# Performance work log

Measured on AMD Instinct MI355X. Metric: run time of the kernel, lower is better.

The kernel has to match this reference:

```python
import jax, jax.numpy as jnp
import numpy as np

N_DETS = 50000
DEG = 32
N_EDGES = N_DETS * DEG

def _xavier(key, fan_in, fan_out):
    lim = np.sqrt(6.0 / (fan_in + fan_out)).astype(np.float32)
    return jax.random.uniform(key, (fan_in, fan_out), jnp.float32, -lim, lim)

def setup_inputs() -> dict:
    key = jax.random.key(0)
    ks = jax.random.split(key, 10)
    detFeatures = jax.random.normal(ks[0], (N_DETS, 128), jnp.float32)
    # every detection has exactly DEG neighbor pairs -> sorted segment ids, no empty segments
    cIdxs = jnp.repeat(jnp.arange(N_DETS, dtype=jnp.int64), DEG)
    nIdxs = jax.random.randint(ks[1], (N_EDGES,), 0, N_DETS, jnp.int64)
    pairFeatures = jax.random.normal(ks[2], (N_EDGES, 32), jnp.float32)
    return {
        "detFeatures": detFeatures,
        "cIdxs": cIdxs,
        "nIdxs": nIdxs,
        "pairFeatures": pairFeatures,
        "W_fc1": _xavier(ks[3], 128, 32), "b_fc1": jnp.zeros((32,), jnp.float32),
        "W_pw1": _xavier(ks[4], 96, 64), "b_pw1": jnp.zeros((64,), jnp.float32),
        "W_pw2": _xavier(ks[5], 64, 64), "b_pw2": jnp.zeros((64,), jnp.float32),
        "W_pm1": _xavier(ks[6], 64, 64), "b_pm1": jnp.zeros((64,), jnp.float32),
        "W_pm2": _xavier(ks[7], 64, 64), "b_pm2": jnp.zeros((64,), jnp.float32),
        "W_out": _xavier(ks[8], 64, 128), "b_out": jnp.zeros((128,), jnp.float32),
    }

def reference(detFeatures, cIdxs, nIdxs, pairFeatures,
              W_fc1, b_fc1, W_pw1, b_pw1, W_pw2, b_pw2,
              W_pm1, b_pm1, W_pm2, b_pm2, W_out, b_out):
    relu = jax.nn.relu
    # fc1: [N,128] -> [N,32]
    h = relu(detFeatures @ W_fc1 + b_fc1)
    # gather center / neighbor feats per pair; zero neighbor feats on identity rows
    cFeats = h[cIdxs]                                   # [E,32]
    nFeats = jnp.where((cIdxs == nIdxs)[:, None], 0.0, h[nIdxs])  # [E,32]
    x = jnp.concatenate((pairFeatures, cFeats, nFeats), axis=1)   # [E,96]
    x = relu(x @ W_pw1 + b_pw1)                         # [E,64]
    x = relu(x @ W_pw2 + b_pw2)                         # [E,64]
    # per-detection segment max (replaces the O(N) python loop)
    m = jax.ops.segment_max(x, cIdxs, num_segments=detFeatures.shape[0])  # [N,64]
    m = relu(m @ W_pm1 + b_pm1)
    m = relu(m @ W_pm2 + b_pm2)
    refined = m @ W_out + b_out                         # [N,128]
    return relu(detFeatures + refined)
```

## Files before the change

### kernel.cpp

```cpp
#include <hip/hip_runtime.h>

#define NDET 50000
#define DEG 32
#define NEDGE (NDET * DEG)
#define NGROUP (NEDGE / 64)

typedef __attribute__((ext_vector_type(8))) short short8;
typedef __attribute__((ext_vector_type(4))) float f32x4;

__device__ inline unsigned short f2bf(float x) {
    return (unsigned short)((__builtin_bit_cast(unsigned int, x) + 0x8000u) >> 16);
}

__device__ inline short8 pack8(f32x4 a, f32x4 b) {
    short8 r;
    r[0] = (short)f2bf(a[0]); r[1] = (short)f2bf(a[1]);
    r[2] = (short)f2bf(a[2]); r[3] = (short)f2bf(a[3]);
    r[4] = (short)f2bf(b[0]); r[5] = (short)f2bf(b[1]);
    r[6] = (short)f2bf(b[2]); r[7] = (short)f2bf(b[3]);
    return r;
}

__global__ __launch_bounds__(256, 4) void fc1_kernel(
    const float* __restrict__ detF,
    const float* __restrict__ W,
    const float* __restrict__ b,
    unsigned short* __restrict__ hbf)
{
    __shared__ __align__(16) unsigned short WT[32 * 136];

    const int tid  = threadIdx.x;
    const int lane = tid & 63;
    const int wv   = tid >> 6;
    const int m16  = lane & 15;
    const int q    = lane >> 4;

    for (int i = tid; i < 32 * 128; i += 256) {
        int n = i >> 7, k = i & 127;
        WT[n * 136 + k] = f2bf(W[k * 32 + n]);
    }
    __syncthreads();

    const int g = blockIdx.x * 4 + wv;
    if (g >= (NDET + 63) / 64) return;
    const int d0 = g * 64;

    f32x4 acc[4][2];
#pragma unroll
    for (int nt = 0; nt < 2; nt++) {
        float c0 = b[nt * 16 + m16];
#pragma unroll
        for (int mt = 0; mt < 4; mt++) acc[mt][nt] = (f32x4){c0, c0, c0, c0};
    }

#pragma unroll
    for (int ks = 0; ks < 4; ks++) {
#pragma unroll
        for (int mt = 0; mt < 4; mt++) {
            int row = d0 + mt * 16 + m16;
            if (row >= NDET) row = NDET - 1;
            const float* pr = detF + (size_t)row * 128 + ks * 32 + q * 8;
            short8 a = pack8(*(const f32x4*)pr, *(const f32x4*)(pr + 4));
#pragma unroll
            for (int nt = 0; nt < 2; nt++) {
                short8 bf = *(const short8*)&WT[(nt * 16 + m16) * 136 + ks * 32 + q * 8];
                acc[mt][nt] = __builtin_amdgcn_mfma_f32_16x16x32_bf16(a, bf, acc[mt][nt], 0, 0, 0);
            }
        }
    }

#pragma unroll
    for (int mt = 0; mt < 4; mt++)
#pragma unroll
        for (int r = 0; r < 4; r++) {
            int row = d0 + mt * 16 + q * 4 + r;
            if (row < NDET) {
#pragma unroll
                for (int nt = 0; nt < 2; nt++)
                    hbf[(size_t)row * 32 + nt * 16 + m16] = f2bf(fmaxf(acc[mt][nt][r], 0.0f));
            }
        }
}

__global__ __launch_bounds__(256, 4) void edge_kernel(
    const unsigned short* __restrict__ hbf,
    const int* __restrict__ nIdx,
    const float* __restrict__ pairF,
    const float* __restrict__ W1,
    const float* __restrict__ b1,
    const float* __restrict__ W2,
    const float* __restrict__ b2,
    unsigned short* __restrict__ m_bf)
{
    __shared__ __align__(16) unsigned short W1T[64 * 104];
    __shared__ __align__(16) unsigned short W2T[64 * 72];
    __shared__ __align__(16) unsigned short Y1s[4][32 * 72];

    const int tid  = threadIdx.x;
    const int lane = tid & 63;
    const int wv   = tid >> 6;
    const int m16  = lane & 15;
    const int q    = lane >> 4;

    for (int i = tid; i < 64 * 96; i += 256) {
        int n = i / 96, k = i - n * 96;
        W1T[n * 104 + k] = f2bf(W1[k * 64 + n]);
    }
    for (int i = tid; i < 64 * 64; i += 256) {
        int n = i >> 6, k = i & 63;
        W2T[n * 72 + k] = f2bf(W2[k * 64 + n]);
    }
    __syncthreads();

    float b1r[4], b2r[4];
#pragma unroll
    for (int nt = 0; nt < 4; nt++) {
        b1r[nt] = b1[nt * 16 + m16];
        b2r[nt] = b2[nt * 16 + m16];
    }

    unsigned short* Y1w = &Y1s[wv][0];

    const int wstride = (int)gridDim.x * 4;
    int g = blockIdx.x * 4 + wv;
    if (g >= NGROUP) return;

    const short8 zr = {0, 0, 0, 0, 0, 0, 0, 0};

    int    ni[4];
    int    sk[4];
    short8 nb[4];

#pragma unroll
    for (int mt = 0; mt < 4; mt++)
        ni[mt] = __builtin_nontemporal_load(&nIdx[g * 64 + mt * 16 + m16]);
#pragma unroll
    for (int mt = 0; mt < 4; mt++) {
        sk[mt] = (ni[mt] == g * 2 + (mt >> 1));
        nb[mt] = *(const short8*)&hbf[(size_t)ni[mt] * 32 + q * 8];
    }
    {
        int g1 = g + wstride;
        int gl = (g1 < NGROUP) ? g1 : g;
#pragma unroll
        for (int mt = 0; mt < 4; mt++)
            ni[mt] = __builtin_nontemporal_load(&nIdx[gl * 64 + mt * 16 + m16]);
    }

    while (true) {
        const int d0 = g * 2;
        const int gn = g + wstride;
        const bool more = (gn < NGROUP);
        const int gt = more ? gn : g;

        f32x4 pv[4][2];
#pragma unroll
        for (int mt = 0; mt < 4; mt++) {
            const float* pr = pairF + (size_t)(g * 64 + mt * 16 + m16) * 32 + q * 8;
            pv[mt][0] = __builtin_nontemporal_load((const f32x4*)pr);
            pv[mt][1] = __builtin_nontemporal_load((const f32x4*)(pr + 4));
        }
        short8 ac2[2];
        ac2[0] = *(const short8*)&hbf[(size_t)d0 * 32 + q * 8];
        ac2[1] = *(const short8*)&hbf[(size_t)(d0 + 1) * 32 + q * 8];

        short8 ap[4], an[4];
#pragma unroll
        for (int mt = 0; mt < 4; mt++) {
            ap[mt] = pack8(pv[mt][0], pv[mt][1]);
            an[mt] = sk[mt] ? zr : nb[mt];
        }

#pragma unroll
        for (int mt = 0; mt < 4; mt++) {
            int s = (ni[mt] == gt * 2 + (mt >> 1));
            nb[mt] = *(const short8*)&hbf[(size_t)ni[mt] * 32 + q * 8];
            sk[mt] = s;
        }
        {
            const int gnn = gn + wstride;
            const int gl2 = (more && gnn < NGROUP) ? gnn : gt;
#pragma unroll
            for (int mt = 0; mt < 4; mt++)
                ni[mt] = __builtin_nontemporal_load(&nIdx[gl2 * 64 + mt * 16 + m16]);
        }

#pragma unroll
        for (int h = 0; h < 2; h++) {
            f32x4 acc[2][4];

#pragma unroll
            for (int j = 0; j < 2; j++)
#pragma unroll
                for (int nt = 0; nt < 4; nt++) {
                    float c0 = b1r[nt];
                    acc[j][nt] = (f32x4){c0, c0, c0, c0};
                }
#pragma unroll
            for (int nt = 0; nt < 4; nt++) {
                const unsigned short* wb = &W1T[(nt * 16 + m16) * 104 + q * 8];
                short8 w0 = *(const short8*)&wb[0];
                acc[0][nt] = __builtin_amdgcn_mfma_f32_16x16x32_bf16(ap[2 * h],     w0, acc[0][nt], 0, 0, 0);
                acc[1][nt] = __builtin_amdgcn_mfma_f32_16x16x32_bf16(ap[2 * h + 1], w0, acc[1][nt], 0, 0, 0);
                short8 w1 = *(const short8*)&wb[64];
                acc[0][nt] = __builtin_amdgcn_mfma_f32_16x16x32_bf16(an[2 * h],     w1, acc[0][nt], 0, 0, 0);
                acc[1][nt] = __builtin_amdgcn_mfma_f32_16x16x32_bf16(an[2 * h + 1], w1, acc[1][nt], 0, 0, 0);
                short8 w2 = *(const short8*)&wb[32];
                acc[0][nt] = __builtin_amdgcn_mfma_f32_16x16x32_bf16(ac2[h], w2, acc[0][nt], 0, 0, 0);
                acc[1][nt] = __builtin_amdgcn_mfma_f32_16x16x32_bf16(ac2[h], w2, acc[1][nt], 0, 0, 0);
            }

#pragma unroll
            for (int j = 0; j < 2; j++)
#pragma unroll
                for (int nt = 0; nt < 4; nt++)
#pragma unroll
                    for (int r = 0; r < 4; r++)
                        Y1w[(j * 16 + q * 4 + r) * 72 + nt * 16 + m16] =
                            f2bf(fmaxf(acc[j][nt][r], 0.0f));

            short8 af0[2], af1[2];
#pragma unroll
            for (int j = 0; j < 2; j++) {
                af0[j] = *(const short8*)&Y1w[(j * 16 + m16) * 72 + q * 8];
                af1[j] = *(const short8*)&Y1w[(j * 16 + m16) * 72 + 32 + q * 8];
            }
#pragma unroll
            for (int j = 0; j < 2; j++)
#pragma unroll
                for (int nt = 0; nt < 4; nt++) {
                    float c0 = b2r[nt];
                    acc[j][nt] = (f32x4){c0, c0, c0, c0};
                }
#pragma unroll
            for (int nt = 0; nt < 4; nt++) {
                short8 wf = *(const short8*)&W2T[(nt * 16 + m16) * 72 + q * 8];
                acc[0][nt] = __builtin_amdgcn_mfma_f32_16x16x32_bf16(af0[0], wf, acc[0][nt], 0, 0, 0);
                acc[1][nt] = __builtin_amdgcn_mfma_f32_16x16x32_bf16(af0[1], wf, acc[1][nt], 0, 0, 0);
                wf = *(const short8*)&W2T[(nt * 16 + m16) * 72 + 32 + q * 8];
                acc[0][nt] = __builtin_amdgcn_mfma_f32_16x16x32_bf16(af1[0], wf, acc[0][nt], 0, 0, 0);
                acc[1][nt] = __builtin_amdgcn_mfma_f32_16x16x32_bf16(af1[1], wf, acc[1][nt], 0, 0, 0);
            }

#pragma unroll
            for (int nt = 0; nt < 4; nt++) {
                float v = 0.0f;
#pragma unroll
                for (int j = 0; j < 2; j++)
#pragma unroll
                    for (int r = 0; r < 4; r++) v = fmaxf(v, acc[j][nt][r]);
                v = fmaxf(v, __shfl_xor(v, 16));
                v = fmaxf(v, __shfl_xor(v, 32));
                if (q == 0) m_bf[(size_t)(d0 + h) * 64 + nt * 16 + m16] = f2bf(v);
            }
        }

        if (!more) break;
        g = gn;
    }
}

__global__ __launch_bounds__(256, 2) void tail_kernel(
    const float* __restrict__ detF,
    const unsigned short* __restrict__ m_bf,
    const float* __restrict__ Wm1, const float* __restrict__ bm1,
    const float* __restrict__ Wm2, const float* __restrict__ bm2,
    const float* __restrict__ Wo,  const float* __restrict__ bo,
    float* __restrict__ out)
{
    __shared__ __align__(16) unsigned short W1T[64 * 72];
    __shared__ __align__(16) unsigned short W2T[64 * 72];
    __shared__ __align__(16) unsigned short WoT[128 * 72];
    __shared__ __align__(16) unsigned short Tt[4][64 * 72];

    const int tid  = threadIdx.x;
    const int lane = tid & 63;
    const int wv   = tid >> 6;
    const int m16  = lane & 15;
    const int q    = lane >> 4;

    for (int i = tid; i < 64 * 64; i += 256) {
        int n = i >> 6, k = i & 63;
        W1T[n * 72 + k] = f2bf(Wm1[k * 64 + n]);
        W2T[n * 72 + k] = f2bf(Wm2[k * 64 + n]);
    }
    for (int i = tid; i < 128 * 64; i += 256) {
        int n = i >> 6, k = i & 63;
        WoT[n * 72 + k] = f2bf(Wo[k * 128 + n]);
    }
    __syncthreads();

    float bm1r[4], bm2r[4], bor[8];
#pragma unroll
    for (int nt = 0; nt < 4; nt++) {
        bm1r[nt] = bm1[nt * 16 + m16];
        bm2r[nt] = bm2[nt * 16 + m16];
    }
#pragma unroll
    for (int nt = 0; nt < 8; nt++) bor[nt] = bo[nt * 16 + m16];

    unsigned short* Tw = &Tt[wv][0];
    const int NTG = (NDET + 63) / 64;

    for (int gI = blockIdx.x * 4 + wv; gI < NTG; gI += (int)gridDim.x * 4) {
        const int d0 = gI * 64;

        f32x4 acc[4][4];
#pragma unroll
        for (int mt = 0; mt < 4; mt++)
#pragma unroll
            for (int nt = 0; nt < 4; nt++) {
                float c0 = bm1r[nt];
                acc[mt][nt] = (f32x4){c0, c0, c0, c0};
            }
#pragma unroll
        for (int ks = 0; ks < 2; ks++) {
            short8 af[4];
#pragma unroll
            for (int mt = 0; mt < 4; mt++) {
                int row = d0 + mt * 16 + m16;
                if (row >= NDET) row = NDET - 1;
                af[mt] = *(const short8*)&m_bf[(size_t)row * 64 + ks * 32 + q * 8];
            }
#pragma unroll
            for (int mt = 0; mt < 4; mt++)
#pragma unroll
                for (int nt = 0; nt < 4; nt++) {
                    short8 bf = *(const short8*)&W1T[(nt * 16 + m16) * 72 + ks * 32 + q * 8];
                    acc[mt][nt] = __builtin_amdgcn_mfma_f32_16x16x32_bf16(af[mt], bf, acc[mt][nt], 0, 0, 0);
                }
        }
#pragma unroll
        for (int mt = 0; mt < 4; mt++)
#pragma unroll
            for (int nt = 0; nt < 4; nt++)
#pragma unroll
                for (int r = 0; r < 4; r++)
                    Tw[(mt * 16 + q * 4 + r) * 72 + nt * 16 + m16] =
                        f2bf(fmaxf(acc[mt][nt][r], 0.0f));

#pragma unroll
        for (int mt = 0; mt < 4; mt++)
#pragma unroll
            for (int nt = 0; nt < 4; nt++) {
                float c0 = bm2r[nt];
                acc[mt][nt] = (f32x4){c0, c0, c0, c0};
            }
#pragma unroll
        for (int ks = 0; ks < 2; ks++) {
            short8 af[4];
#pragma unroll
            for (int mt = 0; mt < 4; mt++)
                af[mt] = *(const short8*)&Tw[(mt * 16 + m16) * 72 + ks * 32 + q * 8];
#pragma unroll
            for (int mt = 0; mt < 4; mt++)
#pragma unroll
                for (int nt = 0; nt < 4; nt++) {
                    short8 bf = *(const short8*)&W2T[(nt * 16 + m16) * 72 + ks * 32 + q * 8];
                    acc[mt][nt] = __builtin_amdgcn_mfma_f32_16x16x32_bf16(af[mt], bf, acc[mt][nt], 0, 0, 0);
                }
        }
#pragma unroll
        for (int mt = 0; mt < 4; mt++)
#pragma unroll
            for (int nt = 0; nt < 4; nt++)
#pragma unroll
                for (int r = 0; r < 4; r++)
                    Tw[(mt * 16 + q * 4 + r) * 72 + nt * 16 + m16] =
                        f2bf(fmaxf(acc[mt][nt][r], 0.0f));

        short8 a3[4][2];
#pragma unroll
        for (int ks = 0; ks < 2; ks++)
#pragma unroll
            for (int mt = 0; mt < 4; mt++)
                a3[mt][ks] = *(const short8*)&Tw[(mt * 16 + m16) * 72 + ks * 32 + q * 8];

#pragma unroll
        for (int h2 = 0; h2 < 2; h2++) {
            f32x4 acc3[4][4];
#pragma unroll
            for (int mt = 0; mt < 4; mt++)
#pragma unroll
                for (int nt = 0; nt < 4; nt++) {
                    float c0 = bor[h2 * 4 + nt];
                    acc3[mt][nt] = (f32x4){c0, c0, c0, c0};
                }
#pragma unroll
            for (int ks = 0; ks < 2; ks++)
#pragma unroll
                for (int mt = 0; mt < 4; mt++)
#pragma unroll
                    for (int nt = 0; nt < 4; nt++) {
                        short8 bf = *(const short8*)&WoT[((h2 * 4 + nt) * 16 + m16) * 72 + ks * 32 + q * 8];
                        acc3[mt][nt] = __builtin_amdgcn_mfma_f32_16x16x32_bf16(a3[mt][ks], bf, acc3[mt][nt], 0, 0, 0);
                    }
#pragma unroll
            for (int mt = 0; mt < 4; mt++)
#pragma unroll
                for (int r = 0; r < 4; r++) {
                    int row = d0 + mt * 16 + q * 4 + r;
                    if (row < NDET) {
#pragma unroll
                        for (int nt = 0; nt < 4; nt++) {
                            int col = (h2 * 4 + nt) * 16 + m16;
                            float v = detF[(size_t)row * 128 + col] + acc3[mt][nt][r];
                            out[(size_t)row * 128 + col] = fmaxf(v, 0.0f);
                        }
                    }
                }
        }
    }
}

extern "C" void kernel_launch(void* const* d_in, const int* in_sizes, int n_in,
                              void* d_out, int out_size, void* d_ws, size_t ws_size,
                              hipStream_t stream)
{
    const float* detF  = (const float*)d_in[0];
    const int*   nIdx  = (const int*)d_in[2];
    const float* pairF = (const float*)d_in[3];
    const float* W_fc1 = (const float*)d_in[4];
    const float* b_fc1 = (const float*)d_in[5];
    const float* W_pw1 = (const float*)d_in[6];
    const float* b_pw1 = (const float*)d_in[7];
    const float* W_pw2 = (const float*)d_in[8];
    const float* b_pw2 = (const float*)d_in[9];
    const float* W_pm1 = (const float*)d_in[10];
    const float* b_pm1 = (const float*)d_in[11];
    const float* W_pm2 = (const float*)d_in[12];
    const float* b_pm2 = (const float*)d_in[13];
    const float* W_out = (const float*)d_in[14];
    const float* b_out = (const float*)d_in[15];
    float* out = (float*)d_out;

    unsigned short* hbf  = (unsigned short*)d_ws;
    unsigned short* m_bf = hbf + (size_t)NDET * 32;

    fc1_kernel<<<(NDET + 255) / 256, 256, 0, stream>>>(detF, W_fc1, b_fc1, hbf);
    edge_kernel<<<1024, 256, 0, stream>>>(hbf, nIdx, pairF,
                                          W_pw1, b_pw1, W_pw2, b_pw2, m_bf);
    tail_kernel<<<256, 256, 0, stream>>>(detF, m_bf, W_pm1, b_pm1, W_pm2, b_pm2,
                                         W_out, b_out, out);
}
```

Baseline: 416.0 us.

## Prefetch pair features one iteration ahead and shrink fc1 tiles to 16 rows

Measured after the change: 499.5 us. 20.1% more time.

```diff
diff --git a/kernel.cpp b/kernel.cpp
--- a/kernel.cpp
+++ b/kernel.cpp
@@ -41,45 +41,35 @@
     }
     __syncthreads();
 
-    const int g = blockIdx.x * 4 + wv;
-    if (g >= (NDET + 63) / 64) return;
-    const int d0 = g * 64;
-
-    f32x4 acc[4][2];
+    const int t = blockIdx.x * 4 + wv;
+    if (t >= NDET / 16) return;
+    const int r0 = t * 16;
+
+    f32x4 acc[2];
 #pragma unroll
     for (int nt = 0; nt < 2; nt++) {
         float c0 = b[nt * 16 + m16];
-#pragma unroll
-        for (int mt = 0; mt < 4; mt++) acc[mt][nt] = (f32x4){c0, c0, c0, c0};
+        acc[nt] = (f32x4){c0, c0, c0, c0};
     }
 
 #pragma unroll
     for (int ks = 0; ks < 4; ks++) {
-#pragma unroll
-        for (int mt = 0; mt < 4; mt++) {
-            int row = d0 + mt * 16 + m16;
-            if (row >= NDET) row = NDET - 1;
-            const float* pr = detF + (size_t)row * 128 + ks * 32 + q * 8;
-            short8 a = pack8(*(const f32x4*)pr, *(const f32x4*)(pr + 4));
-#pragma unroll
-            for (int nt = 0; nt < 2; nt++) {
-                short8 bf = *(const short8*)&WT[(nt * 16 + m16) * 136 + ks * 32 + q * 8];
-                acc[mt][nt] = __builtin_amdgcn_mfma_f32_16x16x32_bf16(a, bf, acc[mt][nt], 0, 0, 0);
-            }
-        }
-    }
-
-#pragma unroll
-    for (int mt = 0; mt < 4; mt++)
-#pragma unroll
-        for (int r = 0; r < 4; r++) {
-            int row = d0 + mt * 16 + q * 4 + r;
-            if (row < NDET) {
-#pragma unroll
-                for (int nt = 0; nt < 2; nt++)
-                    hbf[(size_t)row * 32 + nt * 16 + m16] = f2bf(fmaxf(acc[mt][nt][r], 0.0f));
-            }
-        }
+        const float* pr = detF + (size_t)(r0 + m16) * 128 + ks * 32 + q * 8;
+        short8 a = pack8(*(const f32x4*)pr, *(const f32x4*)(pr + 4));
+#pragma unroll
+        for (int nt = 0; nt < 2; nt++) {
+            short8 bf = *(const short8*)&WT[(nt * 16 + m16) * 136 + ks * 32 + q * 8];
+            acc[nt] = __builtin_amdgcn_mfma_f32_16x16x32_bf16(a, bf, acc[nt], 0, 0, 0);
+        }
+    }
+
+#pragma unroll
+    for (int r = 0; r < 4; r++) {
+        int row = r0 + q * 4 + r;
+#pragma unroll
+        for (int nt = 0; nt < 2; nt++)
+            hbf[(size_t)row * 32 + nt * 16 + m16] = f2bf(fmaxf(acc[nt][r], 0.0f));
+    }
 }
 
 __global__ __launch_bounds__(256, 4) void edge_kernel(
@@ -130,10 +120,17 @@
     int    ni[4];
     int    sk[4];
     short8 nb[4];
+    f32x4  pv[4][2];
 
 #pragma unroll
     for (int mt = 0; mt < 4; mt++)
         ni[mt] = __builtin_nontemporal_load(&nIdx[g * 64 + mt * 16 + m16]);
+#pragma unroll
+    for (int mt = 0; mt < 4; mt++) {
+        const float* pr = pairF + (size_t)(g * 64 + mt * 16 + m16) * 32 + q * 8;
+        pv[mt][0] = __builtin_nontemporal_load((const f32x4*)pr);
+        pv[mt][1] = __builtin_nontemporal_load((const f32x4*)(pr + 4));
+    }
 #pragma unroll
     for (int mt = 0; mt < 4; mt++) {
         sk[mt] = (ni[mt] == g * 2 + (mt >> 1));
@@ -151,39 +148,26 @@
         const int d0 = g * 2;
         const int gn = g + wstride;
         const bool more = (gn < NGROUP);
-        const int gt = more ? gn : g;
-
-        f32x4 pv[4][2];
+        const int gt  = more ? gn : g;
+        const int gnn = gn + wstride;
+        const int gl2 = (more && gnn < NGROUP) ? gnn : gt;
+
+        short8 ap[4];
+#pragma unroll
+        for (int mt = 0; mt < 4; mt++) ap[mt] = pack8(pv[mt][0], pv[mt][1]);
 #pragma unroll
         for (int mt = 0; mt < 4; mt++) {
-            const float* pr = pairF + (size_t)(g * 64 + mt * 16 + m16) * 32 + q * 8;
+            const float* pr = pairF + (size_t)(gt * 64 + mt * 16 + m16) * 32 + q * 8;
             pv[mt][0] = __builtin_nontemporal_load((const f32x4*)pr);
             pv[mt][1] = __builtin_nontemporal_load((const f32x4*)(pr + 4));
         }
+
+#pragma unroll
+        for (int mt = 0; mt < 4; mt++)
+            if (sk[mt]) nb[mt] = zr;
         short8 ac2[2];
         ac2[0] = *(const short8*)&hbf[(size_t)d0 * 32 + q * 8];
         ac2[1] = *(const short8*)&hbf[(size_t)(d0 + 1) * 32 + q * 8];
-
-        short8 ap[4], an[4];
-#pragma unroll
-        for (int mt = 0; mt < 4; mt++) {
-            ap[mt] = pack8(pv[mt][0], pv[mt][1]);
-            an[mt] = sk[mt] ? zr : nb[mt];
-        }
-
-#pragma unroll
-        for (int mt = 0; mt < 4; mt++) {
-            int s = (ni[mt] == gt * 2 + (mt >> 1));
-            nb[mt] = *(const short8*)&hbf[(size_t)ni[mt] * 32 + q * 8];
-            sk[mt] = s;
-        }
-        {
-            const int gnn = gn + wstride;
-            const int gl2 = (more && gnn < NGROUP) ? gnn : gt;
-#pragma unroll
-            for (int mt = 0; mt < 4; mt++)
-                ni[mt] = __builtin_nontemporal_load(&nIdx[gl2 * 64 + mt * 16 + m16]);
-        }
 
 #pragma unroll
         for (int h = 0; h < 2; h++) {
@@ -203,11 +187,21 @@
                 acc[0][nt] = __builtin_amdgcn_mfma_f32_16x16x32_bf16(ap[2 * h],     w0, acc[0][nt], 0, 0, 0);
                 acc[1][nt] = __builtin_amdgcn_mfma_f32_16x16x32_bf16(ap[2 * h + 1], w0, acc[1][nt], 0, 0, 0);
                 short8 w1 = *(const short8*)&wb[64];
-                acc[0][nt] = __builtin_amdgcn_mfma_f32_16x16x32_bf16(an[2 * h],     w1, acc[0][nt], 0, 0, 0);
-                acc[1][nt] = __builtin_amdgcn_mfma_f32_16x16x32_bf16(an[2 * h + 1], w1, acc[1][nt], 0, 0, 0);
+                acc[0][nt] = __builtin_amdgcn_mfma_f32_16x16x32_bf16(nb[2 * h],     w1, acc[0][nt], 0, 0, 0);
+                acc[1][nt] = __builtin_amdgcn_mfma_f32_16x16x32_bf16(nb[2 * h + 1], w1, acc[1][nt], 0, 0, 0);
                 short8 w2 = *(const short8*)&wb[32];
                 acc[0][nt] = __builtin_amdgcn_mfma_f32_16x16x32_bf16(ac2[h], w2, acc[0][nt], 0, 0, 0);
                 acc[1][nt] = __builtin_amdgcn_mfma_f32_16x16x32_bf16(ac2[h], w2, acc[1][nt], 0, 0, 0);
+            }
+
+            {
+                const int m0 = 2 * h, m1 = 2 * h + 1;
+                nb[m0] = *(const short8*)&hbf[(size_t)ni[m0] * 32 + q * 8];
+                sk[m0] = (ni[m0] == gt * 2 + h);
+                nb[m1] = *(const short8*)&hbf[(size_t)ni[m1] * 32 + q * 8];
+                sk[m1] = (ni[m1] == gt * 2 + h);
+                ni[m0] = __builtin_nontemporal_load(&nIdx[gl2 * 64 + m0 * 16 + m16]);
+                ni[m1] = __builtin_nontemporal_load(&nIdx[gl2 * 64 + m1 * 16 + m16]);
             }
 
 #pragma unroll
@@ -437,7 +431,7 @@
     unsigned short* hbf  = (unsigned short*)d_ws;
     unsigned short* m_bf = hbf + (size_t)NDET * 32;
 
-    fc1_kernel<<<(NDET + 255) / 256, 256, 0, stream>>>(detF, W_fc1, b_fc1, hbf);
+    fc1_kernel<<<(NDET / 16 + 3) / 4, 256, 0, stream>>>(detF, W_fc1, b_fc1, hbf);
     edge_kernel<<<1024, 256, 0, stream>>>(hbf, nIdx, pairF,
                                           W_pw1, b_pw1, W_pw2, b_pw2, m_bf);
     tail_kernel<<<256, 256, 0, stream>>>(detF, m_bf, W_pm1, b_pm1, W_pm2, b_pm2,
```
